# Optimization experiments

Hardware: AMD Instinct MI355X
Metric: run time of the kernel (lower is better)

The kernel has to match this reference:

```python
import jax, jax.numpy as jnp
import numpy as np

B, T_IN, H, V, MAXLEN = 128, 256, 512, 32, 128


def gru_cell(x, h, Wih, Whh, bih, bhh):
    # torch GRU cell: gates ordered (r, z, n)
    gi = x @ Wih.T + bih            # [B, 3H]
    gh = h @ Whh.T + bhh            # [B, 3H]
    ir, iz, inn = jnp.split(gi, 3, axis=-1)
    hr, hz, hn = jnp.split(gh, 3, axis=-1)
    r = jax.nn.sigmoid(ir + hr)
    z = jax.nn.sigmoid(iz + hz)
    n = jnp.tanh(inn + r * hn)
    return (1.0 - z) * n + z * h


def run_gru_layer(xs, Wih, Whh, bih, bhh):
    # xs: [B, T, D] -> outputs [B, T, H], final hidden [B, H]
    h0 = jnp.zeros((xs.shape[0], Whh.shape[1]), xs.dtype)

    def step(h, x):
        hn = gru_cell(x, h, Wih, Whh, bih, bhh)
        return hn, hn

    hT, ys = jax.lax.scan(step, h0, jnp.swapaxes(xs, 0, 1))
    return jnp.swapaxes(ys, 0, 1), hT


def setup_inputs() -> dict:
    key = jax.random.key(0)
    ks = jax.random.split(key, 24)
    s = 1.0 / np.sqrt(H)

    def p(k, shape):
        return (jax.random.normal(k, shape, jnp.float32) * s).astype(jnp.float32)

    return {
        "x": jax.random.normal(ks[0], (B, T_IN, 2), jnp.float32),
        "emb": p(ks[1], (V, H)),
        # encoder GRU: layer0 input dim 2, layer1 input dim H
        "enc_Wih0": p(ks[2], (3 * H, 2)), "enc_Whh0": p(ks[3], (3 * H, H)),
        "enc_bih0": p(ks[4], (3 * H,)), "enc_bhh0": p(ks[5], (3 * H,)),
        "enc_Wih1": p(ks[6], (3 * H, H)), "enc_Whh1": p(ks[7], (3 * H, H)),
        "enc_bih1": p(ks[8], (3 * H,)), "enc_bhh1": p(ks[9], (3 * H,)),
        # decoder GRU: layer0 input dim 2H (embedded+context), layer1 input dim H
        "dec_Wih0": p(ks[10], (3 * H, 2 * H)), "dec_Whh0": p(ks[11], (3 * H, H)),
        "dec_bih0": p(ks[12], (3 * H,)), "dec_bhh0": p(ks[13], (3 * H,)),
        "dec_Wih1": p(ks[14], (3 * H, H)), "dec_Whh1": p(ks[15], (3 * H, H)),
        "dec_bih1": p(ks[16], (3 * H,)), "dec_bhh1": p(ks[17], (3 * H,)),
        "q_W": p(ks[18], (H, H)), "q_b": p(ks[19], (H,)),
        "out_W": p(ks[20], (V, H)), "out_b": p(ks[21], (V,)),
    }


def reference(x, emb,
              enc_Wih0, enc_Whh0, enc_bih0, enc_bhh0,
              enc_Wih1, enc_Whh1, enc_bih1, enc_bhh1,
              dec_Wih0, dec_Whh0, dec_bih0, dec_bhh0,
              dec_Wih1, dec_Whh1, dec_bih1, dec_bhh1,
              q_W, q_b, out_W, out_b):
    # ----- encoder: 2-layer GRU over trajectory points -----
    y0, h0 = run_gru_layer(x, enc_Wih0, enc_Whh0, enc_bih0, enc_bhh0)
    enc_outs, h1 = run_gru_layer(y0, enc_Wih1, enc_Whh1, enc_bih1, enc_bhh1)
    hidden0 = jnp.stack([h0, h1])                      # [L, B, H]
    bsz = x.shape[0]

    def step(carry, _):
        hidden, tok = carry                            # [L,B,H], [B] int
        embedded = emb[tok]                            # [B, H]
        query = hidden[-1] @ q_W.T + q_b               # [B, H]
        scores = jnp.einsum('bh,bth->bt', query, enc_outs)
        attn_w = jax.nn.softmax(scores, axis=-1)       # [B, T_in]
        context = jnp.einsum('bt,bth->bh', attn_w, enc_outs)
        rnn_in = jnp.concatenate([embedded, context], axis=-1)  # [B, 2H]
        g0 = gru_cell(rnn_in, hidden[0], dec_Wih0, dec_Whh0, dec_bih0, dec_bhh0)
        g1 = gru_cell(g0, hidden[1], dec_Wih1, dec_Whh1, dec_bih1, dec_bhh1)
        logits = g1 @ out_W.T + out_b                  # [B, V]
        tok_next = jnp.argmax(logits, axis=-1)
        return (jnp.stack([g0, g1]), tok_next), (logits, attn_w)

    tok0 = jnp.zeros((bsz,), jnp.int32)
    (hidden_f, _), (logits_seq, attn_seq) = jax.lax.scan(
        step, (hidden0, tok0), None, length=MAXLEN)
    vec_out = jnp.swapaxes(logits_seq, 0, 1)           # [B, max_len, V]
    attn = jnp.swapaxes(attn_seq, 0, 1)                # [B, max_len, T_in]
    return vec_out, hidden_f, attn
```

## Files before the change

### kernel.cpp

```cpp
#include <hip/hip_runtime.h>
#include <math.h>

#define BB 128
#define TT 256
#define HH 512
#define VV 32
#define MLEN 128
#define SLOT 65536

#define WT_OFF 0
#define QT_OFF 24576
#define PR_OFF 26624
#define SC_OFF 28416
#define SM_FLOATS 32512

#define HX(d, b) ((((d) >> 1) << 8) + ((b) << 1) + ((d) & 1))
#define SX(t, b) ((((t) >> 1) << 8) + ((b) << 1) + ((t) & 1))
#define EX(t, j, b) ((ll)(t) * (HH * BB) + (((j) >> 1) << 8) + ((b) << 1) + ((j) & 1))

typedef long long ll;

struct P {
    const float *x, *emb;
    const float *eWih0, *eWhh0, *ebih0, *ebhh0;
    const float *eWih1, *eWhh1, *ebih1, *ebhh1;
    const float *dWih0, *dWhh0, *dbih0, *dbhh0;
    const float *dWih1, *dWhh1, *dbih1, *dbhh1;
    const float *qW, *qb, *outW, *outb;
    float *ws;
    float *vecO, *hidO, *attnO;
};

__device__ __forceinline__ float sigf(float v) { return 1.0f / (1.0f + __expf(-v)); }

__device__ __forceinline__ float ldA(const float* p) {
    return __hip_atomic_load(p, __ATOMIC_RELAXED, __HIP_MEMORY_SCOPE_AGENT);
}
__device__ __forceinline__ float2 ldA2(const float* p) {
    unsigned long long v = __hip_atomic_load((const unsigned long long*)p,
                                             __ATOMIC_RELAXED, __HIP_MEMORY_SCOPE_AGENT);
    union { unsigned long long u; float2 f; } c; c.u = v; return c.f;
}
__device__ __forceinline__ void stA(float* p, float v) {
    __hip_atomic_store(p, v, __ATOMIC_RELAXED, __HIP_MEMORY_SCOPE_AGENT);
}
__device__ __forceinline__ int ldAi(const int* p) {
    return __hip_atomic_load(p, __ATOMIC_RELAXED, __HIP_MEMORY_SCOPE_AGENT);
}
__device__ __forceinline__ void stAi(int* p, int v) {
    __hip_atomic_store(p, v, __ATOMIC_RELAXED, __HIP_MEMORY_SCOPE_AGENT);
}

__device__ __forceinline__ void gbar(int* W, int target) {
    __syncthreads();
    if (threadIdx.x == 0) {
        int par = target & 1;
        int g = blockIdx.x & 15;
        int* gc = W + 32 + (par * 16 + g) * 32;
        if (__hip_atomic_fetch_add(gc, 1, __ATOMIC_RELAXED, __HIP_MEMORY_SCOPE_AGENT) == 15) {
            __hip_atomic_store(gc, 0, __ATOMIC_RELAXED, __HIP_MEMORY_SCOPE_AGENT);
            int* rc = W + 1056 + par * 32;
            if (__hip_atomic_fetch_add(rc, 1, __ATOMIC_RELAXED, __HIP_MEMORY_SCOPE_AGENT) == 15) {
                __hip_atomic_store(rc, 0, __ATOMIC_RELAXED, __HIP_MEMORY_SCOPE_AGENT);
                __hip_atomic_store(W, target, __ATOMIC_RELAXED, __HIP_MEMORY_SCOPE_AGENT);
            }
        }
        while (__hip_atomic_load(W, __ATOMIC_RELAXED, __HIP_MEMORY_SCOPE_AGENT) < target)
            __builtin_amdgcn_s_sleep(2);
    }
    __syncthreads();
}

__global__ __launch_bounds__(512, 1) void kmain(P p) {
    __shared__ __align__(16) float smu[SM_FLOATS];
    const int tid = threadIdx.x;
    const int lane = tid & 63;
    const int wv = tid >> 6;
    const int blk = blockIdx.x;

    int* W = (int*)p.ws;
    int* tok = W + 4096;
    float* f = (float*)p.ws + 8192;
    float* eh0 = f;
    float* eh1 = f + 2 * SLOT;
    float* inp = f + 4 * SLOT;
    float* qbm = f + 5 * SLOT;
    float* scoresB = f + 6 * SLOT;
    float* T = f + 6 * SLOT + SLOT / 2;
    float* xT = T + 3 * HH * VV;
    float* encO = f + (SLOT / 4) * 33;

    const float4* t4 = (const float4*)smu;
    const float4* t4q = (const float4*)(smu + QT_OFF);

    const int jg = blk >> 1;
    const int bh = blk & 1;
    const int b2 = bh * 64 + lane;
    int bar = 0;

    {
        stA(eh0 + blk * 1024 + tid, 0.0f);
        stA(eh0 + blk * 1024 + 512 + tid, 0.0f);
        if (tid < 256) {
            int idx = blk * 256 + tid;
            int t = idx >> 8, c = (idx >> 7) & 1, b = idx & 127;
            stA(xT + idx, p.x[((ll)b * TT + t) * 2 + c]);
        }
        if (tid < 192) {
            int unit = blk * 192 + tid;
            int v = unit & 31, gj = unit >> 5;
            const float* wrow = p.dWih0 + (ll)gj * 1024;
            const float* erow = p.emb + (ll)v * HH;
            float acc = 0.0f;
#pragma unroll 8
            for (int d = 0; d < HH; ++d) acc = fmaf(wrow[d], erow[d], acc);
            stA(T + unit, acc);
        }
#pragma unroll
        for (int jl = 0; jl < 4; ++jl)
            smu[QT_OFF + jl * 512 + tid] = p.qW[((ll)(jg * 4 + jl)) * HH + tid];
#pragma unroll
        for (int r = 0; r < 24; ++r) {
            int g = r >> 2, jl = r & 3, j = jg * 4 + jl;
            const float* src = (g < 3) ? (p.eWhh0 + (ll)(g * HH + j) * HH)
                                       : (p.eWih1 + (ll)((g - 3) * HH + j) * HH);
            smu[WT_OFF + r * 512 + tid] = src[tid];
        }
#pragma unroll
        for (int r = 0; r < 12; ++r) {
            int g = r >> 2, jl = r & 3, j = jg * 4 + jl;
            smu[WT_OFF + (24 + r) * 512 + tid] = p.eWhh1[(ll)(g * HH + j) * HH + tid];
        }
        gbar(W, ++bar);
    }

    for (int t = 0; t <= TT; ++t) {
        const float* h0s = eh0 + (((t + 1) & 1) ? SLOT : 0);
        float*       h0d = eh0 + ((t & 1) ? SLOT : 0);
        const float* h1s = eh1 + (((t + 1) & 1) ? SLOT : 0);
        float*       h1d = eh1 + ((t & 1) ? SLOT : 0);

        smu[PR_OFF + tid] = 0.0f;
        smu[PR_OFF + 512 + tid] = 0.0f;
        smu[PR_OFF + 1024 + tid] = 0.0f;
        if (tid < 256) smu[PR_OFF + 1536 + tid] = 0.0f;
        __syncthreads();

        {
            const int rotE = jg & 7;
            const int ds0 = wv * 64;
            float acc[36];
#pragma unroll
            for (int r = 0; r < 36; ++r) acc[r] = 0.0f;
            float av[2][8], bv[2][8];
            {
                const int d0c = ds0 + rotE * 8;
#pragma unroll
                for (int k = 0; k < 4; ++k) {
                    float2 va = ldA2(h0s + HX(d0c + 2 * k, b2));
                    av[0][2 * k] = va.x; av[0][2 * k + 1] = va.y;
                    float2 vb = ldA2(h1s + HX(d0c + 2 * k, b2));
                    bv[0][2 * k] = vb.x; bv[0][2 * k + 1] = vb.y;
                }
            }
#pragma unroll
            for (int c = 0; c < 8; ++c) {
                const int cb = c & 1, pb = cb ^ 1;
                if (c < 7) {
                    const int dn = ds0 + ((c + 1 + rotE) & 7) * 8;
#pragma unroll
                    for (int k = 0; k < 4; ++k) {
                        float2 va = ldA2(h0s + HX(dn + 2 * k, b2));
                        av[pb][2 * k] = va.x; av[pb][2 * k + 1] = va.y;
                        float2 vb = ldA2(h1s + HX(dn + 2 * k, b2));
                        bv[pb][2 * k] = vb.x; bv[pb][2 * k + 1] = vb.y;
                    }
                }
                const int db = ds0 + ((c + rotE) & 7) * 8;
#pragma unroll
                for (int h2 = 0; h2 < 2; ++h2) {
                    const int q4 = (db + h2 * 4) >> 2;
#pragma unroll
                    for (int r = 0; r < 24; ++r) {
                        float4 w = t4[r * 128 + q4];
                        acc[r] = fmaf(w.x, av[cb][h2 * 4 + 0], acc[r]);
                        acc[r] = fmaf(w.y, av[cb][h2 * 4 + 1], acc[r]);
                        acc[r] = fmaf(w.z, av[cb][h2 * 4 + 2], acc[r]);
                        acc[r] = fmaf(w.w, av[cb][h2 * 4 + 3], acc[r]);
                    }
#pragma unroll
                    for (int r = 0; r < 12; ++r) {
                        float4 w = t4[(24 + r) * 128 + q4];
                        acc[24 + r] = fmaf(w.x, bv[cb][h2 * 4 + 0], acc[24 + r]);
                        acc[24 + r] = fmaf(w.y, bv[cb][h2 * 4 + 1], acc[24 + r]);
                        acc[24 + r] = fmaf(w.z, bv[cb][h2 * 4 + 2], acc[24 + r]);
                        acc[24 + r] = fmaf(w.w, bv[cb][h2 * 4 + 3], acc[24 + r]);
                    }
                }
            }
#pragma unroll
            for (int r = 0; r < 24; ++r)
                unsafeAtomicAdd(&smu[PR_OFF + r * 64 + lane], acc[r]);
#pragma unroll
            for (int r = 0; r < 12; ++r) {
                int g = r >> 2;
                int prow = (g < 2) ? (12 + g * 4) : 24;
                unsafeAtomicAdd(&smu[PR_OFF + (prow + (r & 3)) * 64 + lane], acc[24 + r]);
            }
        }
        __syncthreads();

        if (wv < 4) {
            if (t < TT) {
                int jl = wv, j = jg * 4 + jl;
                float* pr = smu + PR_OFF;
                float hr = pr[(0 + jl) * 64 + lane] + p.ebhh0[j];
                float hz = pr[(4 + jl) * 64 + lane] + p.ebhh0[HH + j];
                float hn = pr[(8 + jl) * 64 + lane] + p.ebhh0[2 * HH + j];
                float x0 = xT[t * 256 + b2], x1 = xT[t * 256 + 128 + b2];
                float ir = fmaf(p.eWih0[j * 2], x0, fmaf(p.eWih0[j * 2 + 1], x1, p.ebih0[j]));
                float iz = fmaf(p.eWih0[(HH + j) * 2], x0, fmaf(p.eWih0[(HH + j) * 2 + 1], x1, p.ebih0[HH + j]));
                float in_ = fmaf(p.eWih0[(2 * HH + j) * 2], x0, fmaf(p.eWih0[(2 * HH + j) * 2 + 1], x1, p.ebih0[2 * HH + j]));
                float r = sigf(ir + hr), z = sigf(iz + hz);
                float n = tanhf(in_ + r * hn);
                float hp = ldA(h0s + HX(j, b2));
                stA(h0d + HX(j, b2), (1.0f - z) * n + z * hp);
            }
        } else if (t >= 1) {
            int jl = wv - 4, j = jg * 4 + jl;
            float* pr = smu + PR_OFF;
            float rs = pr[(12 + jl) * 64 + lane] + p.ebih1[j] + p.ebhh1[j];
            float zs = pr[(16 + jl) * 64 + lane] + p.ebih1[HH + j] + p.ebhh1[HH + j];
            float in1 = pr[(20 + jl) * 64 + lane] + p.ebih1[2 * HH + j];
            float hn1 = pr[(24 + jl) * 64 + lane] + p.ebhh1[2 * HH + j];
            float r = sigf(rs), z = sigf(zs);
            float n = tanhf(in1 + r * hn1);
            float hp = ldA(h1s + HX(j, b2));
            float hv = (1.0f - z) * n + z * hp;
            stA(h1d + HX(j, b2), hv);
            stA(encO + EX(t - 1, j, b2), hv);
        }
        gbar(W, ++bar);
    }

    {
        const float* h1c = eh1;
        if (tid < 256) smu[PR_OFF + tid] = 0.0f;
#pragma unroll
        for (int r = 0; r < 12; ++r) {
            int g = r >> 2, jl = r & 3, j = jg * 4 + jl;
            smu[WT_OFF + r * 1024 + tid]              = p.dWih0[(ll)(g * HH + j) * 1024 + 512 + tid];
            smu[WT_OFF + r * 1024 + 512 + tid]        = p.dWhh0[(ll)(g * HH + j) * HH + tid];
            smu[WT_OFF + (12 + r) * 1024 + tid]       = p.dWih1[(ll)(g * HH + j) * HH + tid];
            smu[WT_OFF + (12 + r) * 1024 + 512 + tid] = p.dWhh1[(ll)(g * HH + j) * HH + tid];
        }
        __syncthreads();
        {
            const int ds0 = wv * 64;
            float acc[4] = {0, 0, 0, 0};
            float av[8];
            for (int c = 0; c < 8; ++c) {
                int db = ds0 + c * 8;
#pragma unroll
                for (int k = 0; k < 4; ++k) {
                    float2 v = ldA2(h1c + HX(db + 2 * k, b2));
                    av[2 * k] = v.x; av[2 * k + 1] = v.y;
                }
#pragma unroll
                for (int h2 = 0; h2 < 2; ++h2) {
                    int q4 = (db + h2 * 4) >> 2;
#pragma unroll
                    for (int jl = 0; jl < 4; ++jl) {
                        float4 w = t4q[jl * 128 + q4];
                        acc[jl] = fmaf(w.x, av[h2 * 4 + 0], acc[jl]);
                        acc[jl] = fmaf(w.y, av[h2 * 4 + 1], acc[jl]);
                        acc[jl] = fmaf(w.z, av[h2 * 4 + 2], acc[jl]);
                        acc[jl] = fmaf(w.w, av[h2 * 4 + 3], acc[jl]);
                    }
                }
            }
#pragma unroll
            for (int jl = 0; jl < 4; ++jl)
                unsafeAtomicAdd(&smu[PR_OFF + jl * 64 + lane], acc[jl]);
        }
        __syncthreads();
        if (wv < 4) {
            int j = jg * 4 + wv;
            stA(qbm + HX(j, b2), smu[PR_OFF + wv * 64 + lane] + p.qb[j]);
        }
        if (blk == 128 && tid < BB) stAi(tok + tid, 0);
        gbar(W, ++bar);
    }

    for (int s = 0; s < MLEN; ++s) {
        const float* h0s = eh0 + (((s + 1) & 1) ? SLOT : 0);
        float*       g0d = eh0 + ((s & 1) ? SLOT : 0);
        const float* h1s = eh1 + ((s & 1) ? SLOT : 0);
        float*       h1d = eh1 + (((s + 1) & 1) ? SLOT : 0);

        {
            const int rotA = jg & 7;
            const int t0 = (blk >> 1) * 2;
            if (tid < 128) smu[PR_OFF + tid] = 0.0f;
            __syncthreads();
            const int js = wv * 64;
            float a0 = 0.0f, a1 = 0.0f;
            float qv[2][8], e0[2][8], e1[2][8];
            {
                const int j0 = js + rotA * 8;
                const float* eb0 = encO + (ll)t0 * (HH * BB) + ((j0 >> 1) << 8) + (b2 << 1);
                const float* eb1 = encO + (ll)(t0 + 1) * (HH * BB) + ((j0 >> 1) << 8) + (b2 << 1);
#pragma unroll
                for (int k = 0; k < 4; ++k) {
                    float2 q2 = ldA2(qbm + HX(j0 + 2 * k, b2));
                    qv[0][2 * k] = q2.x; qv[0][2 * k + 1] = q2.y;
                    float2 v0 = *(const float2*)(eb0 + k * 256);
                    e0[0][2 * k] = v0.x; e0[0][2 * k + 1] = v0.y;
                    float2 v1 = *(const float2*)(eb1 + k * 256);
                    e1[0][2 * k] = v1.x; e1[0][2 * k + 1] = v1.y;
                }
            }
#pragma unroll
            for (int c = 0; c < 8; ++c) {
                const int cb = c & 1, pb = cb ^ 1;
                if (c < 7) {
                    const int jn = js + ((c + 1 + rotA) & 7) * 8;
                    const float* eb0 = encO + (ll)t0 * (HH * BB) + ((jn >> 1) << 8) + (b2 << 1);
                    const float* eb1 = encO + (ll)(t0 + 1) * (HH * BB) + ((jn >> 1) << 8) + (b2 << 1);
#pragma unroll
                    for (int k = 0; k < 4; ++k) {
                        float2 q2 = ldA2(qbm + HX(jn + 2 * k, b2));
                        qv[pb][2 * k] = q2.x; qv[pb][2 * k + 1] = q2.y;
                        float2 v0 = *(const float2*)(eb0 + k * 256);
                        e0[pb][2 * k] = v0.x; e0[pb][2 * k + 1] = v0.y;
                        float2 v1 = *(const float2*)(eb1 + k * 256);
                        e1[pb][2 * k] = v1.x; e1[pb][2 * k + 1] = v1.y;
                    }
                }
#pragma unroll
                for (int u = 0; u < 8; ++u) {
                    a0 = fmaf(qv[cb][u], e0[cb][u], a0);
                    a1 = fmaf(qv[cb][u], e1[cb][u], a1);
                }
            }
            unsafeAtomicAdd(&smu[PR_OFF + lane], a0);
            unsafeAtomicAdd(&smu[PR_OFF + 64 + lane], a1);
            __syncthreads();
            if (wv < 2)
                stA(scoresB + SX(t0 + wv, b2), smu[PR_OFF + wv * 64 + lane]);
        }
        gbar(W, ++bar);

        {
            const int d0 = jg * 4;
            float sv[32];
#pragma unroll
            for (int kp = 0; kp < 16; ++kp) {
                float2 v = ldA2(scoresB + ((wv * 16 + kp) << 8) + (b2 << 1));
                sv[2 * kp] = v.x; sv[2 * kp + 1] = v.y;
            }
            if (tid < 256) smu[PR_OFF + tid] = 0.0f;
            float mp = sv[0];
#pragma unroll
            for (int k = 1; k < 32; ++k) mp = fmaxf(mp, sv[k]);
            smu[SC_OFF + wv * 64 + lane] = mp;
            __syncthreads();
            float m = smu[SC_OFF + lane];
#pragma unroll
            for (int u = 1; u < 8; ++u) m = fmaxf(m, smu[SC_OFF + u * 64 + lane]);
            float e[32], lp = 0.0f;
#pragma unroll
            for (int k = 0; k < 32; ++k) { e[k] = __expf(sv[k] - m); lp += e[k]; }
            smu[SC_OFF + 512 + wv * 64 + lane] = lp;
            __syncthreads();
            float l = smu[SC_OFF + 512 + lane];
#pragma unroll
            for (int u = 1; u < 8; ++u) l += smu[SC_OFF + 512 + u * 64 + lane];
            float rl = 1.0f / l;
            if (blk < 16 && wv == jg) {
#pragma unroll
                for (int k = 0; k < 32; ++k) smu[SC_OFF + 1024 + k * 65 + lane] = e[k] * rl;
            }
            float c4[4] = {0, 0, 0, 0};
            float ev[2][32];
#pragma unroll
            for (int u = 0; u < 8; ++u) {
                const float* Ep = encO + (ll)(wv * 32 + u) * (HH * BB) + ((d0 >> 1) << 8) + (b2 << 1);
                float2 pa = *(const float2*)(Ep);
                float2 pb2 = *(const float2*)(Ep + 256);
                ev[0][u * 4 + 0] = pa.x; ev[0][u * 4 + 1] = pa.y;
                ev[0][u * 4 + 2] = pb2.x; ev[0][u * 4 + 3] = pb2.y;
            }
#pragma unroll
            for (int kb = 0; kb < 4; ++kb) {
                const int cb = kb & 1, pb = cb ^ 1;
                if (kb < 3) {
#pragma unroll
                    for (int u = 0; u < 8; ++u) {
                        const float* Ep = encO + (ll)(wv * 32 + (kb + 1) * 8 + u) * (HH * BB) + ((d0 >> 1) << 8) + (b2 << 1);
                        float2 pa = *(const float2*)(Ep);
                        float2 pb2 = *(const float2*)(Ep + 256);
                        ev[pb][u * 4 + 0] = pa.x; ev[pb][u * 4 + 1] = pa.y;
                        ev[pb][u * 4 + 2] = pb2.x; ev[pb][u * 4 + 3] = pb2.y;
                    }
                }
#pragma unroll
                for (int u = 0; u < 8; ++u) {
                    const int k = kb * 8 + u;
                    c4[0] = fmaf(e[k], ev[cb][u * 4 + 0], c4[0]);
                    c4[1] = fmaf(e[k], ev[cb][u * 4 + 1], c4[1]);
                    c4[2] = fmaf(e[k], ev[cb][u * 4 + 2], c4[2]);
                    c4[3] = fmaf(e[k], ev[cb][u * 4 + 3], c4[3]);
                }
            }
#pragma unroll
            for (int kk = 0; kk < 4; ++kk)
                unsafeAtomicAdd(&smu[PR_OFF + kk * 64 + lane], c4[kk]);
            __syncthreads();
            if (tid < 256) {
                int kk = tid >> 6, ln = tid & 63;
                float l2 = smu[SC_OFF + 512 + ln];
#pragma unroll
                for (int u = 1; u < 8; ++u) l2 += smu[SC_OFF + 512 + u * 64 + ln];
                float val = smu[PR_OFF + kk * 64 + ln] / l2;
                stA(inp + HX(d0 + kk, bh * 64 + ln), val);
            }
            if (blk < 16) {
                int bi = tid >> 3, tj = tid & 7;
#pragma unroll
                for (int u = 0; u < 4; ++u) {
                    int tl = tj * 4 + u;
                    p.attnO[((ll)(bh * 64 + bi) * MLEN + s) * TT + jg * 32 + tl] = smu[SC_OFF + 1024 + tl * 65 + bi];
                }
            }
        }
        gbar(W, ++bar);

        {
            const int rotG = jg & 15;
            smu[PR_OFF + tid] = 0.0f;
            smu[PR_OFF + 512 + tid] = 0.0f;
            __syncthreads();
            const int ctxw = (wv < 4);
            const float* stream = ctxw ? inp : h0s;
            const int ds0 = (wv & 3) * 128;
            const int tb = ctxw ? 0 : 512;
            float acc[12];
#pragma unroll
            for (int r = 0; r < 12; ++r) acc[r] = 0.0f;
            float av[2][8];
            {
                const int d0c = ds0 + rotG * 8;
#pragma unroll
                for (int k = 0; k < 4; ++k) {
                    float2 v = ldA2(stream + HX(d0c + 2 * k, b2));
                    av[0][2 * k] = v.x; av[0][2 * k + 1] = v.y;
                }
            }
#pragma unroll
            for (int c = 0; c < 16; ++c) {
                const int cb = c & 1, pb = cb ^ 1;
                if (c < 15) {
                    const int dn = ds0 + ((c + 1 + rotG) & 15) * 8;
#pragma unroll
                    for (int k = 0; k < 4; ++k) {
                        float2 v = ldA2(stream + HX(dn + 2 * k, b2));
                        av[pb][2 * k] = v.x; av[pb][2 * k + 1] = v.y;
                    }
                }
                const int db = ds0 + ((c + rotG) & 15) * 8;
#pragma unroll
                for (int h2 = 0; h2 < 2; ++h2) {
                    const int q4 = (tb + db + h2 * 4) >> 2;
#pragma unroll
                    for (int r = 0; r < 12; ++r) {
                        float4 w = t4[r * 256 + q4];
                        acc[r] = fmaf(w.x, av[cb][h2 * 4 + 0], acc[r]);
                        acc[r] = fmaf(w.y, av[cb][h2 * 4 + 1], acc[r]);
                        acc[r] = fmaf(w.z, av[cb][h2 * 4 + 2], acc[r]);
                        acc[r] = fmaf(w.w, av[cb][h2 * 4 + 3], acc[r]);
                    }
                }
            }
#pragma unroll
            for (int r = 0; r < 12; ++r) {
                int g = r >> 2;
                int prow = (g < 2) ? g * 4 : (ctxw ? 8 : 12);
                unsafeAtomicAdd(&smu[PR_OFF + (prow + (r & 3)) * 64 + lane], acc[r]);
            }
            __syncthreads();
            if (wv < 4) {
                int jl = wv, j = jg * 4 + jl;
                float* pr = smu + PR_OFF;
                int tokb = ldAi(tok + b2);
                float rs = T[(ll)j * 32 + tokb] + pr[(0 + jl) * 64 + lane] + p.dbih0[j] + p.dbhh0[j];
                float zs = T[(ll)(HH + j) * 32 + tokb] + pr[(4 + jl) * 64 + lane] + p.dbih0[HH + j] + p.dbhh0[HH + j];
                float ins = T[(ll)(2 * HH + j) * 32 + tokb] + pr[(8 + jl) * 64 + lane] + p.dbih0[2 * HH + j];
                float hns = pr[(12 + jl) * 64 + lane] + p.dbhh0[2 * HH + j];
                float r = sigf(rs), z = sigf(zs);
                float n = tanhf(ins + r * hns);
                float hp = ldA(h0s + HX(j, b2));
                stA(g0d + HX(j, b2), (1.0f - z) * n + z * hp);
            }
        }
        gbar(W, ++bar);

        {
            const int rotG = jg & 15;
            smu[PR_OFF + tid] = 0.0f;
            smu[PR_OFF + 512 + tid] = 0.0f;
            __syncthreads();
            const int iw = (wv < 4);
            const float* stream = iw ? g0d : h1s;
            const int ds0 = (wv & 3) * 128;
            const int tb = iw ? 0 : 512;
            float acc[12];
#pragma unroll
            for (int r = 0; r < 12; ++r) acc[r] = 0.0f;
            float av[2][8];
            {
                const int d0c = ds0 + rotG * 8;
#pragma unroll
                for (int k = 0; k < 4; ++k) {
                    float2 v = ldA2(stream + HX(d0c + 2 * k, b2));
                    av[0][2 * k] = v.x; av[0][2 * k + 1] = v.y;
                }
            }
#pragma unroll
            for (int c = 0; c < 16; ++c) {
                const int cb = c & 1, pb = cb ^ 1;
                if (c < 15) {
                    const int dn = ds0 + ((c + 1 + rotG) & 15) * 8;
#pragma unroll
                    for (int k = 0; k < 4; ++k) {
                        float2 v = ldA2(stream + HX(dn + 2 * k, b2));
                        av[pb][2 * k] = v.x; av[pb][2 * k + 1] = v.y;
                    }
                }
                const int db = ds0 + ((c + rotG) & 15) * 8;
#pragma unroll
                for (int h2 = 0; h2 < 2; ++h2) {
                    const int q4 = (tb + db + h2 * 4) >> 2;
#pragma unroll
                    for (int r = 0; r < 12; ++r) {
                        float4 w = t4[(12 + r) * 256 + q4];
                        acc[r] = fmaf(w.x, av[cb][h2 * 4 + 0], acc[r]);
                        acc[r] = fmaf(w.y, av[cb][h2 * 4 + 1], acc[r]);
                        acc[r] = fmaf(w.z, av[cb][h2 * 4 + 2], acc[r]);
                        acc[r] = fmaf(w.w, av[cb][h2 * 4 + 3], acc[r]);
                    }
                }
            }
#pragma unroll
            for (int r = 0; r < 12; ++r) {
                int g = r >> 2;
                int prow = (g < 2) ? g * 4 : (iw ? 8 : 12);
                unsafeAtomicAdd(&smu[PR_OFF + (prow + (r & 3)) * 64 + lane], acc[r]);
            }
            __syncthreads();
            if (wv < 4) {
                int jl = wv, j = jg * 4 + jl;
                float* pr = smu + PR_OFF;
                float rs = pr[(0 + jl) * 64 + lane] + p.dbih1[j] + p.dbhh1[j];
                float zs = pr[(4 + jl) * 64 + lane] + p.dbih1[HH + j] + p.dbhh1[HH + j];
                float ins = pr[(8 + jl) * 64 + lane] + p.dbih1[2 * HH + j];
                float hns = pr[(12 + jl) * 64 + lane] + p.dbhh1[2 * HH + j];
                float r = sigf(rs), z = sigf(zs);
                float n = tanhf(ins + r * hns);
                float hp = ldA(h1s + HX(j, b2));
                stA(h1d + HX(j, b2), (1.0f - z) * n + z * hp);
            }
        }
        gbar(W, ++bar);

        {
            const int rotD = jg & 7;
            const float* h1c = h1d;
            if (tid < 256) smu[PR_OFF + tid] = 0.0f;
            __syncthreads();
            {
                const int ds0 = wv * 64;
                float acc4[4] = {0, 0, 0, 0};
                float av[2][8];
                {
                    const int d0c = ds0 + rotD * 8;
#pragma unroll
                    for (int k = 0; k < 4; ++k) {
                        float2 v = ldA2(h1c + HX(d0c + 2 * k, b2));
                        av[0][2 * k] = v.x; av[0][2 * k + 1] = v.y;
                    }
                }
#pragma unroll
                for (int c = 0; c < 8; ++c) {
                    const int cb = c & 1, pb = cb ^ 1;
                    if (c < 7) {
                        const int dn = ds0 + ((c + 1 + rotD) & 7) * 8;
#pragma unroll
                        for (int k = 0; k < 4; ++k) {
                            float2 v = ldA2(h1c + HX(dn + 2 * k, b2));
                            av[pb][2 * k] = v.x; av[pb][2 * k + 1] = v.y;
                        }
                    }
                    const int db = ds0 + ((c + rotD) & 7) * 8;
#pragma unroll
                    for (int h2 = 0; h2 < 2; ++h2) {
                        const int q4 = (db + h2 * 4) >> 2;
#pragma unroll
                        for (int jl = 0; jl < 4; ++jl) {
                            float4 w = t4q[jl * 128 + q4];
                            acc4[jl] = fmaf(w.x, av[cb][h2 * 4 + 0], acc4[jl]);
                            acc4[jl] = fmaf(w.y, av[cb][h2 * 4 + 1], acc4[jl]);
                            acc4[jl] = fmaf(w.z, av[cb][h2 * 4 + 2], acc4[jl]);
                            acc4[jl] = fmaf(w.w, av[cb][h2 * 4 + 3], acc4[jl]);
                        }
                    }
                }
#pragma unroll
                for (int jl = 0; jl < 4; ++jl)
                    unsafeAtomicAdd(&smu[PR_OFF + jl * 64 + lane], acc4[jl]);
            }
            __syncthreads();
            if (wv < 4) {
                int j = jg * 4 + wv;
                stA(qbm + HX(j, b2), smu[PR_OFF + wv * 64 + lane] + p.qb[j]);
            }
            if (blk >= 128 && blk < 160) {
                __syncthreads();
                const int bb = (blk - 128) * 4;
#pragma unroll
                for (int i = 0; i < 4; ++i) {
                    int f2 = i * 512 + tid;
                    int d = f2 >> 2, bi2 = f2 & 3;
                    smu[SC_OFF + f2] = ldA(h1c + HX(d, bb + bi2));
                }
                __syncthreads();
                if (tid < 128) {
                    const int bl = tid >> 5, v = tid & 31;
                    float acc = 0.0f;
                    for (int d4 = 0; d4 < 128; ++d4) {
                        float4 w4 = *(const float4*)(p.outW + (ll)v * HH + d4 * 4);
                        acc = fmaf(w4.x, smu[SC_OFF + (d4 * 4 + 0) * 4 + bl], acc);
                        acc = fmaf(w4.y, smu[SC_OFF + (d4 * 4 + 1) * 4 + bl], acc);
                        acc = fmaf(w4.z, smu[SC_OFF + (d4 * 4 + 2) * 4 + bl], acc);
                        acc = fmaf(w4.w, smu[SC_OFF + (d4 * 4 + 3) * 4 + bl], acc);
                    }
                    acc += p.outb[v];
                    p.vecO[((ll)(bb + bl) * MLEN + s) * VV + v] = acc;
                    smu[SC_OFF + 2048 + tid] = acc;
                }
                __syncthreads();
                if (tid < 4) {
                    int base = SC_OFF + 2048 + tid * 32;
                    float best = smu[base];
                    int bi2 = 0;
#pragma unroll
                    for (int u = 1; u < 32; ++u) {
                        float val = smu[base + u];
                        if (val > best) { best = val; bi2 = u; }
                    }
                    stAi(tok + bb + tid, bi2);
                }
            }
        }
        gbar(W, ++bar);
    }

    {
        int idx = blk * 512 + tid;
        int l = idx >> 16, rr = idx & 65535;
        int b = rr >> 9, h = rr & 511;
        const float* src = l ? eh1 : (eh0 + SLOT);
        p.hidO[idx] = ldA(src + HX(h, b));
    }
}

extern "C" void kernel_launch(void* const* d_in, const int* in_sizes, int n_in,
                              void* d_out, int out_size, void* d_ws, size_t ws_size,
                              hipStream_t stream) {
    (void)in_sizes; (void)n_in; (void)out_size; (void)ws_size;
    P prm;
    prm.x     = (const float*)d_in[0];
    prm.emb   = (const float*)d_in[1];
    prm.eWih0 = (const float*)d_in[2];
    prm.eWhh0 = (const float*)d_in[3];
    prm.ebih0 = (const float*)d_in[4];
    prm.ebhh0 = (const float*)d_in[5];
    prm.eWih1 = (const float*)d_in[6];
    prm.eWhh1 = (const float*)d_in[7];
    prm.ebih1 = (const float*)d_in[8];
    prm.ebhh1 = (const float*)d_in[9];
    prm.dWih0 = (const float*)d_in[10];
    prm.dWhh0 = (const float*)d_in[11];
    prm.dbih0 = (const float*)d_in[12];
    prm.dbhh0 = (const float*)d_in[13];
    prm.dWih1 = (const float*)d_in[14];
    prm.dWhh1 = (const float*)d_in[15];
    prm.dbih1 = (const float*)d_in[16];
    prm.dbhh1 = (const float*)d_in[17];
    prm.qW    = (const float*)d_in[18];
    prm.qb    = (const float*)d_in[19];
    prm.outW  = (const float*)d_in[20];
    prm.outb  = (const float*)d_in[21];
    prm.ws    = (float*)d_ws;
    prm.vecO  = (float*)d_out;
    prm.hidO  = prm.vecO + (ll)BB * MLEN * VV;
    prm.attnO = prm.hidO + (ll)2 * BB * HH;

    hipMemsetAsync(d_ws, 0, 16384, stream);
    void* args[] = { &prm };
    hipLaunchCooperativeKernel((void*)kmain, dim3(256), dim3(512), args, 0, stream);
}
```

Baseline: 29.45 ms.

## Precompute qW-projected encoder outputs and fold output projection into attention phase

Uses the identity score = (h1·qW^T + qb)·enc = h1·(qW^T·enc) + qb·enc. The projected encoder outputs and a bias term are precomputed once after the encoder, so each decoder step no longer needs the query matmul. The output-logit/argmax for step s-1 is moved into the attention phase of step s, which removes one grid barrier per decoder step. In exchange it needs a large extra workspace (a second encoder-sized buffer) and a one-off precompute pass that reads qW transposed from global memory, and it falls back to the old path if the workspace is too small.

Measured after the change: 29.44 ms. About the same (-0.0%).

```diff
diff --git a/kernel.cpp b/kernel.cpp
--- a/kernel.cpp
+++ b/kernel.cpp
@@ -16,9 +16,13 @@
 
 #define HX(d, b) ((((d) >> 1) << 8) + ((b) << 1) + ((d) & 1))
 #define SX(t, b) ((((t) >> 1) << 8) + ((b) << 1) + ((t) & 1))
-#define EX(t, j, b) ((ll)(t) * (HH * BB) + (((j) >> 1) << 8) + ((b) << 1) + ((j) & 1))
 
 typedef long long ll;
+
+#define PM_OFF   17317888LL
+#define QWT_OFF  (PM_OFF + 16777216LL)
+#define CT_OFF   (QWT_OFF + 262144LL)
+#define WS_NEED  ((8192LL + CT_OFF + 32768LL) * 4)
 
 struct P {
     const float *x, *emb;
@@ -71,6 +75,7 @@
     __syncthreads();
 }
 
+template<int PM>
 __global__ __launch_bounds__(512, 1) void kmain(P p) {
     __shared__ __align__(16) float smu[SM_FLOATS];
     const int tid = threadIdx.x;
@@ -89,6 +94,9 @@
     float* T = f + 6 * SLOT + SLOT / 2;
     float* xT = T + 3 * HH * VV;
     float* encO = f + (SLOT / 4) * 33;
+    float* Pm  = f + PM_OFF;
+    float* qWTp = f + QWT_OFF;
+    float* cTp  = f + CT_OFF;
 
     const float4* t4 = (const float4*)smu;
     const float4* t4q = (const float4*)(smu + QT_OFF);
@@ -115,6 +123,14 @@
 #pragma unroll 8
             for (int d = 0; d < HH; ++d) acc = fmaf(wrow[d], erow[d], acc);
             stA(T + unit, acc);
+        }
+        if constexpr (PM) {
+#pragma unroll
+            for (int r = 0; r < 2; ++r) {
+                int k = blk * 1024 + r * 512 + tid;
+                int d = k >> 9, j = k & 511;
+                stA(qWTp + k, p.qW[(ll)j * HH + d]);
+            }
         }
 #pragma unroll
         for (int jl = 0; jl < 4; ++jl)
@@ -238,13 +254,12 @@
             float hp = ldA(h1s + HX(j, b2));
             float hv = (1.0f - z) * n + z * hp;
             stA(h1d + HX(j, b2), hv);
-            stA(encO + EX(t - 1, j, b2), hv);
+            stA(encO + (ll)(t - 1) * (HH * BB) + HX(j, b2), hv);
         }
         gbar(W, ++bar);
     }
 
     {
-        const float* h1c = eh1;
         if (tid < 256) smu[PR_OFF + tid] = 0.0f;
 #pragma unroll
         for (int r = 0; r < 12; ++r) {
@@ -255,7 +270,8 @@
             smu[WT_OFF + (12 + r) * 1024 + 512 + tid] = p.dWhh1[(ll)(g * HH + j) * HH + tid];
         }
         __syncthreads();
-        {
+        if constexpr (!PM) {
+            const float* h1c = eh1;
             const int ds0 = wv * 64;
             float acc[4] = {0, 0, 0, 0};
             float av[8];
@@ -282,11 +298,67 @@
 #pragma unroll
             for (int jl = 0; jl < 4; ++jl)
                 unsafeAtomicAdd(&smu[PR_OFF + jl * 64 + lane], acc[jl]);
-        }
-        __syncthreads();
-        if (wv < 4) {
-            int j = jg * 4 + wv;
-            stA(qbm + HX(j, b2), smu[PR_OFF + wv * 64 + lane] + p.qb[j]);
+            __syncthreads();
+            if (wv < 4) {
+                int j = jg * 4 + wv;
+                stA(qbm + HX(j, b2), smu[PR_OFF + wv * 64 + lane] + p.qb[j]);
+            }
+        } else {
+            const int t0p = (blk >> 1) * 2;
+#pragma unroll 1
+            for (int tt = 0; tt < 2; ++tt) {
+                const int t = t0p + tt;
+                const float* Eb = encO + (ll)t * (HH * BB) + (b2 << 1);
+                float* Pb = Pm + (ll)t * (HH * BB);
+#pragma unroll 1
+                for (int dc = 0; dc < 8; ++dc) {
+                    const int dbase = wv * 64 + dc * 8;
+                    float acc8[8];
+#pragma unroll
+                    for (int u = 0; u < 8; ++u) acc8[u] = 0.0f;
+                    const float2* q0 = (const float2*)(qWTp + (ll)(dbase + 0) * HH);
+                    const float2* q1 = (const float2*)(qWTp + (ll)(dbase + 1) * HH);
+                    const float2* q2p = (const float2*)(qWTp + (ll)(dbase + 2) * HH);
+                    const float2* q3 = (const float2*)(qWTp + (ll)(dbase + 3) * HH);
+                    const float2* q4p = (const float2*)(qWTp + (ll)(dbase + 4) * HH);
+                    const float2* q5 = (const float2*)(qWTp + (ll)(dbase + 5) * HH);
+                    const float2* q6 = (const float2*)(qWTp + (ll)(dbase + 6) * HH);
+                    const float2* q7 = (const float2*)(qWTp + (ll)(dbase + 7) * HH);
+#pragma unroll 4
+                    for (int jp = 0; jp < 256; ++jp) {
+                        float2 e2 = *(const float2*)(Eb + (jp << 8));
+                        float2 w;
+                        w = q0[jp]; acc8[0] = fmaf(w.x, e2.x, fmaf(w.y, e2.y, acc8[0]));
+                        w = q1[jp]; acc8[1] = fmaf(w.x, e2.x, fmaf(w.y, e2.y, acc8[1]));
+                        w = q2p[jp]; acc8[2] = fmaf(w.x, e2.x, fmaf(w.y, e2.y, acc8[2]));
+                        w = q3[jp]; acc8[3] = fmaf(w.x, e2.x, fmaf(w.y, e2.y, acc8[3]));
+                        w = q4p[jp]; acc8[4] = fmaf(w.x, e2.x, fmaf(w.y, e2.y, acc8[4]));
+                        w = q5[jp]; acc8[5] = fmaf(w.x, e2.x, fmaf(w.y, e2.y, acc8[5]));
+                        w = q6[jp]; acc8[6] = fmaf(w.x, e2.x, fmaf(w.y, e2.y, acc8[6]));
+                        w = q7[jp]; acc8[7] = fmaf(w.x, e2.x, fmaf(w.y, e2.y, acc8[7]));
+                    }
+#pragma unroll
+                    for (int u = 0; u < 8; ++u) {
+                        int d = dbase + u;
+                        stA(Pb + HX(d, b2), acc8[u]);
+                    }
+                }
+            }
+            if (wv == 0) {
+#pragma unroll 1
+                for (int tt = 0; tt < 2; ++tt) {
+                    const int t = t0p + tt;
+                    const float* Eb = encO + (ll)t * (HH * BB) + (b2 << 1);
+                    float acc = 0.0f;
+#pragma unroll 4
+                    for (int jp = 0; jp < 256; ++jp) {
+                        float2 e2 = *(const float2*)(Eb + (jp << 8));
+                        float2 qv2 = *(const float2*)(p.qb + jp * 2);
+                        acc = fmaf(qv2.x, e2.x, fmaf(qv2.y, e2.y, acc));
+                    }
+                    stA(cTp + SX(t, b2), acc);
+                }
+            }
         }
         if (blk == 128 && tid < BB) stAi(tok + tid, 0);
         gbar(W, ++bar);
@@ -306,13 +378,16 @@
             const int js = wv * 64;
             float a0 = 0.0f, a1 = 0.0f;
             float qv[2][8], e0[2][8], e1[2][8];
+            const float* S0 = PM ? (Pm + (ll)t0 * (HH * BB)) : (encO + (ll)t0 * (HH * BB));
+            const float* S1 = PM ? (Pm + (ll)(t0 + 1) * (HH * BB)) : (encO + (ll)(t0 + 1) * (HH * BB));
+            const float* Qs = PM ? h1s : qbm;
             {
                 const int j0 = js + rotA * 8;
-                const float* eb0 = encO + (ll)t0 * (HH * BB) + ((j0 >> 1) << 8) + (b2 << 1);
-                const float* eb1 = encO + (ll)(t0 + 1) * (HH * BB) + ((j0 >> 1) << 8) + (b2 << 1);
+                const float* eb0 = S0 + ((j0 >> 1) << 8) + (b2 << 1);
+                const float* eb1 = S1 + ((j0 >> 1) << 8) + (b2 << 1);
 #pragma unroll
                 for (int k = 0; k < 4; ++k) {
-                    float2 q2 = ldA2(qbm + HX(j0 + 2 * k, b2));
+                    float2 q2 = ldA2(Qs + HX(j0 + 2 * k, b2));
                     qv[0][2 * k] = q2.x; qv[0][2 * k + 1] = q2.y;
                     float2 v0 = *(const float2*)(eb0 + k * 256);
                     e0[0][2 * k] = v0.x; e0[0][2 * k + 1] = v0.y;
@@ -325,11 +400,11 @@
                 const int cb = c & 1, pb = cb ^ 1;
                 if (c < 7) {
                     const int jn = js + ((c + 1 + rotA) & 7) * 8;
-                    const float* eb0 = encO + (ll)t0 * (HH * BB) + ((jn >> 1) << 8) + (b2 << 1);
-                    const float* eb1 = encO + (ll)(t0 + 1) * (HH * BB) + ((jn >> 1) << 8) + (b2 << 1);
+                    const float* eb0 = S0 + ((jn >> 1) << 8) + (b2 << 1);
+                    const float* eb1 = S1 + ((jn >> 1) << 8) + (b2 << 1);
 #pragma unroll
                     for (int k = 0; k < 4; ++k) {
-                        float2 q2 = ldA2(qbm + HX(jn + 2 * k, b2));
+                        float2 q2 = ldA2(Qs + HX(jn + 2 * k, b2));
                         qv[pb][2 * k] = q2.x; qv[pb][2 * k + 1] = q2.y;
                         float2 v0 = *(const float2*)(eb0 + k * 256);
                         e0[pb][2 * k] = v0.x; e0[pb][2 * k + 1] = v0.y;
@@ -346,8 +421,50 @@
             unsafeAtomicAdd(&smu[PR_OFF + lane], a0);
             unsafeAtomicAdd(&smu[PR_OFF + 64 + lane], a1);
             __syncthreads();
-            if (wv < 2)
-                stA(scoresB + SX(t0 + wv, b2), smu[PR_OFF + wv * 64 + lane]);
+            if (wv < 2) {
+                float base = smu[PR_OFF + wv * 64 + lane];
+                if constexpr (PM) base += cTp[SX(t0 + wv, b2)];
+                stA(scoresB + SX(t0 + wv, b2), base);
+            }
+            if constexpr (PM) {
+                if (blk >= 128 && blk < 160 && s >= 1) {
+                    __syncthreads();
+                    const int bb = (blk - 128) * 4;
+#pragma unroll
+                    for (int i = 0; i < 4; ++i) {
+                        int f2 = i * 512 + tid;
+                        int d = f2 >> 2, bi2 = f2 & 3;
+                        smu[SC_OFF + f2] = ldA(h1s + HX(d, bb + bi2));
+                    }
+                    __syncthreads();
+                    if (tid < 128) {
+                        const int bl = tid >> 5, v = tid & 31;
+                        float acc = 0.0f;
+                        for (int d4 = 0; d4 < 128; ++d4) {
+                            float4 w4 = *(const float4*)(p.outW + (ll)v * HH + d4 * 4);
+                            acc = fmaf(w4.x, smu[SC_OFF + (d4 * 4 + 0) * 4 + bl], acc);
+                            acc = fmaf(w4.y, smu[SC_OFF + (d4 * 4 + 1) * 4 + bl], acc);
+                            acc = fmaf(w4.z, smu[SC_OFF + (d4 * 4 + 2) * 4 + bl], acc);
+                            acc = fmaf(w4.w, smu[SC_OFF + (d4 * 4 + 3) * 4 + bl], acc);
+                        }
+                        acc += p.outb[v];
+                        p.vecO[((ll)(bb + bl) * MLEN + (s - 1)) * VV + v] = acc;
+                        smu[SC_OFF + 2048 + tid] = acc;
+                    }
+                    __syncthreads();
+                    if (tid < 4) {
+                        int base = SC_OFF + 2048 + tid * 32;
+                        float best = smu[base];
+                        int bi2 = 0;
+#pragma unroll
+                        for (int u = 1; u < 32; ++u) {
+                            float val = smu[base + u];
+                            if (val > best) { best = val; bi2 = u; }
+                        }
+                        stAi(tok + bb + tid, bi2);
+                    }
+                }
+            }
         }
         gbar(W, ++bar);
 
@@ -573,7 +690,7 @@
         }
         gbar(W, ++bar);
 
-        {
+        if constexpr (!PM) {
             const int rotD = jg & 7;
             const float* h1c = h1d;
             if (tid < 256) smu[PR_OFF + tid] = 0.0f;
@@ -661,8 +778,36 @@
                     stAi(tok + bb + tid, bi2);
                 }
             }
-        }
-        gbar(W, ++bar);
+            gbar(W, ++bar);
+        }
+    }
+
+    if constexpr (PM) {
+        if (blk >= 128 && blk < 160) {
+            const float* h1c = eh1;
+            const int bb = (blk - 128) * 4;
+            __syncthreads();
+#pragma unroll
+            for (int i = 0; i < 4; ++i) {
+                int f2 = i * 512 + tid;
+                int d = f2 >> 2, bi2 = f2 & 3;
+                smu[SC_OFF + f2] = ldA(h1c + HX(d, bb + bi2));
+            }
+            __syncthreads();
+            if (tid < 128) {
+                const int bl = tid >> 5, v = tid & 31;
+                float acc = 0.0f;
+                for (int d4 = 0; d4 < 128; ++d4) {
+                    float4 w4 = *(const float4*)(p.outW + (ll)v * HH + d4 * 4);
+                    acc = fmaf(w4.x, smu[SC_OFF + (d4 * 4 + 0) * 4 + bl], acc);
+                    acc = fmaf(w4.y, smu[SC_OFF + (d4 * 4 + 1) * 4 + bl], acc);
+                    acc = fmaf(w4.z, smu[SC_OFF + (d4 * 4 + 2) * 4 + bl], acc);
+                    acc = fmaf(w4.w, smu[SC_OFF + (d4 * 4 + 3) * 4 + bl], acc);
+                }
+                acc += p.outb[v];
+                p.vecO[((ll)(bb + bl) * MLEN + (MLEN - 1)) * VV + v] = acc;
+            }
+        }
     }
 
     {
@@ -677,7 +822,7 @@
 extern "C" void kernel_launch(void* const* d_in, const int* in_sizes, int n_in,
                               void* d_out, int out_size, void* d_ws, size_t ws_size,
                               hipStream_t stream) {
-    (void)in_sizes; (void)n_in; (void)out_size; (void)ws_size;
+    (void)in_sizes; (void)n_in; (void)out_size;
     P prm;
     prm.x     = (const float*)d_in[0];
     prm.emb   = (const float*)d_in[1];
@@ -708,5 +853,9 @@
 
     hipMemsetAsync(d_ws, 0, 16384, stream);
     void* args[] = { &prm };
-    hipLaunchCooperativeKernel((void*)kmain, dim3(256), dim3(512), args, 0, stream);
+    if (ws_size >= (size_t)WS_NEED) {
+        hipLaunchCooperativeKernel((void*)kmain<1>, dim3(256), dim3(512), args, 0, stream);
+    } else {
+        hipLaunchCooperativeKernel((void*)kmain<0>, dim3(256), dim3(512), args, 0, stream);
+    }
 }
```
